# Kernel tuning notes

Measured on AMD Instinct MI355X. Metric: run time of the kernel, lower is better.

## Reference

```python
import jax, jax.numpy as jnp
import numpy as np

KW = 3          # kernel_width
PAD = (KW - 1) // 2


def setup_inputs() -> dict:
    key = jax.random.key(0)
    ks = jax.random.split(key, 7)
    B, Lq, Lk, D, C = 8, 1024, 1024, 512, 512  # D=q_size, C=k_size
    return {
        "q": jax.random.normal(ks[0], (B, Lq, D), jnp.float32),
        "k": jax.random.normal(ks[1], (B, Lk, C), jnp.float32),
        "W_kernel": jax.random.normal(ks[2], (D, C * KW), jnp.float32) * (1.0 / np.sqrt(D)),
        "b_kernel": jax.random.normal(ks[3], (C * KW,), jnp.float32) * 0.02,
        "W_bias": jax.random.normal(ks[4], (D, 1), jnp.float32) * (1.0 / np.sqrt(D)),
        "b_bias": jax.random.normal(ks[5], (1,), jnp.float32) * 0.02,
        "bias_b": jax.random.normal(ks[6], (1,), jnp.float32),
    }


def reference(q, k, W_kernel, b_kernel, W_bias, b_bias, bias_b):
    B, Lq, D = q.shape
    _, Lk, C = k.shape
    # per-(batch, query) dynamic conv kernels: [B, Lq, C, KW]
    kernel = (q @ W_kernel + b_kernel).reshape(B, Lq, C, KW)
    # per-(batch, query) scalar bias: [B, Lq]
    bias = (q @ W_bias + b_bias)[..., 0]
    # windowed view of k (cross-correlation with 'same' padding)
    kpad = jnp.pad(k, ((0, 0), (PAD, PAD), (0, 0)))  # [B, Lk+2*PAD, C]
    win_idx = jnp.arange(Lk)[:, None] + jnp.arange(KW)[None, :]  # [Lk, KW]
    kwin = kpad[:, win_idx, :]  # [B, Lk, KW, C]
    # a[b,i,j] = sum_{c,w} kernel[b,i,c,w] * kpad[b, j+w, c] + bias[b,i] + bias_b
    a_ij = jnp.einsum('bicw,bjwc->bij', kernel, kwin)
    return a_ij + bias[:, :, None] + bias_b
```

## Files before the change

kernel.cpp:

```cpp
#include <hip/hip_runtime.h>


typedef __attribute__((ext_vector_type(8))) short s8vec;
typedef __attribute__((ext_vector_type(4))) float floatx4;

__device__ __forceinline__ unsigned short f2bf(float f) {
    union { float f; unsigned u; } v; v.f = f;
    unsigned r = (v.u + 0x7FFFu + ((v.u >> 16) & 1u)) >> 16;
    return (unsigned short)r;
}

__device__ __forceinline__ void gl2lds16(const void* g, void* l) {
    __builtin_amdgcn_global_load_lds(
        (__attribute__((address_space(1))) void*)(g),
        (__attribute__((address_space(3))) void*)(l), 16, 0, 0);
}

__global__ void cvt_all(const float* __restrict__ q, const float* __restrict__ k,
                        unsigned short* __restrict__ qbf, unsigned short* __restrict__ kp,
                        const float* __restrict__ Wb, const float* __restrict__ b_bias,
                        float* __restrict__ biasb,
                        const float* __restrict__ W, unsigned short* __restrict__ Wt) {
    int blk = blockIdx.x;
    if (blk < 4104) {
        int t = blk * 256 + threadIdx.x;
        if (t < 524288) {
            const float4* p = (const float4*)q + 2 * (size_t)t;
            float4 a = p[0], b = p[1];
            union { unsigned short s[8]; uint4 v; } o;
            o.s[0]=f2bf(a.x); o.s[1]=f2bf(a.y); o.s[2]=f2bf(a.z); o.s[3]=f2bf(a.w);
            o.s[4]=f2bf(b.x); o.s[5]=f2bf(b.y); o.s[6]=f2bf(b.z); o.s[7]=f2bf(b.w);
            ((uint4*)qbf)[t] = o.v;
        } else if (t < 1048576) {
            int e8 = t - 524288;
            size_t e = (size_t)e8 * 8;
            int b = e8 >> 16;
            int j = (e8 >> 6) & 1023;
            int c = (e8 & 63) * 8;
            const float4* p = (const float4*)(k + e);
            float4 a = p[0], bb = p[1];
            union { unsigned short s[8]; uint4 v; } o;
            o.s[0]=f2bf(a.x); o.s[1]=f2bf(a.y); o.s[2]=f2bf(a.z); o.s[3]=f2bf(a.w);
            o.s[4]=f2bf(bb.x); o.s[5]=f2bf(bb.y); o.s[6]=f2bf(bb.z); o.s[7]=f2bf(bb.w);
            *(uint4*)(kp + ((size_t)(b * 1028 + j + 1) * 512 + c)) = o.v;
        } else if (t < 1050624) {
            int z = t - 1048576;
            int b = z >> 8, r = (z >> 6) & 3, ch = z & 63;
            int row = r ? (1024 + r) : 0;
            *(uint4*)(kp + ((size_t)(b * 1028 + row) * 512 + ch * 8)) = make_uint4(0u,0u,0u,0u);
        }
    } else if (blk < 6152) {
        int row  = (blk - 4104) * 4 + (threadIdx.x >> 6);
        int lane = threadIdx.x & 63;
        const float4* qr = (const float4*)(q + (size_t)row * 512) + lane * 2;
        const float4* wb = (const float4*)Wb + lane * 2;
        float4 a0 = qr[0], a1 = qr[1], b0 = wb[0], b1 = wb[1];
        float s = a0.x*b0.x + a0.y*b0.y + a0.z*b0.z + a0.w*b0.w
                + a1.x*b1.x + a1.y*b1.y + a1.z*b1.z + a1.w*b1.w;
        #pragma unroll
        for (int off = 32; off > 0; off >>= 1) s += __shfl_down(s, off);
        if (lane == 0) biasb[row] = s + b_bias[0];
    } else {
        __shared__ float lds[32][33];
        int p = blk - 6152;
        int cw0 = (p % 48) * 32, d0 = (p / 48) * 32;
        int tid = threadIdx.x;
        #pragma unroll
        for (int rep = 0; rep < 4; rep++) {
            int e = rep * 256 + tid, dy = e >> 5, dx = e & 31;
            lds[dy][dx] = W[(size_t)(d0 + dy) * 1536 + cw0 + dx];
        }
        __syncthreads();
        #pragma unroll
        for (int rep = 0; rep < 4; rep++) {
            int e = rep * 256 + tid, cy = e >> 5, cx = e & 31;
            int cw = cw0 + cy, c = cw / 3, w = cw % 3;
            Wt[((size_t)(w * 512 + c)) * 512 + d0 + cx] = f2bf(lds[cx][cy]);
        }
    }
}

__global__ __launch_bounds__(256) void gemm_A(const unsigned short* __restrict__ Abf,
                                              const unsigned short* __restrict__ Bbf,
                                              const float* __restrict__ b_kernel,
                                              unsigned short* __restrict__ G) {
    __shared__ unsigned short lds_a[128 * 32];
    __shared__ unsigned short lds_b[128 * 32];
    int g = blockIdx.x;
    int xcd = g & 7, slot = g >> 3;
    int n_blk = slot / 8;
    int i_blk = xcd * 8 + (slot & 7);
    int i0 = i_blk * 128;
    int n0 = n_blk * 128;
    int tid = threadIdx.x, wid = tid >> 6, lane = tid & 63;
    int wm = wid >> 1, wn = wid & 1;
    floatx4 acc[4][4] = {};

    for (int kk = 0; kk < 512; kk += 32) {
        #pragma unroll
        for (int s = 0; s < 2; ++s) {
            int t = wid * 2 + s;
            const unsigned short* ga = Abf + (size_t)(i0 + t * 16 + (lane >> 2)) * 512 + kk + (lane & 3) * 8;
            gl2lds16(ga, (char*)lds_a + t * 1024);
            const unsigned short* gb = Bbf + (size_t)(n0 + t * 16 + (lane >> 2)) * 512 + kk + (lane & 3) * 8;
            gl2lds16(gb, (char*)lds_b + t * 1024);
        }
        __syncthreads();
        int ra = lane & 15, q8 = (lane >> 4) * 8;
        s8vec af[4], bf_[4];
        #pragma unroll
        for (int mi = 0; mi < 4; mi++)
            af[mi] = *(const s8vec*)(lds_a + (wm * 64 + mi * 16 + ra) * 32 + q8);
        #pragma unroll
        for (int ni = 0; ni < 4; ni++)
            bf_[ni] = *(const s8vec*)(lds_b + (wn * 64 + ni * 16 + ra) * 32 + q8);
        #pragma unroll
        for (int mi = 0; mi < 4; mi++)
            #pragma unroll
            for (int ni = 0; ni < 4; ni++)
                acc[mi][ni] = __builtin_amdgcn_mfma_f32_16x16x32_bf16(af[mi], bf_[ni], acc[mi][ni], 0, 0, 0);
        __syncthreads();
    }

    int cl = lane & 15, qd = lane >> 4;
    #pragma unroll
    for (int mi = 0; mi < 4; mi++) {
        #pragma unroll
        for (int ni = 0; ni < 4; ni++) {
            int n_all = n0 + wn * 64 + ni * 16 + cl;
            int c = n_all & 511, w = n_all >> 9;
            float bk = b_kernel[c * 3 + w];
            #pragma unroll
            for (int r = 0; r < 4; r++) {
                int i_g = i0 + wm * 64 + mi * 16 + qd * 4 + r;
                int b = i_g >> 10, ii = i_g & 1023;
                G[((size_t)((b * 3 + w) * 1024 + ii)) * 512 + c] = f2bf(acc[mi][ni][r] + bk);
            }
        }
    }
}

__global__ __launch_bounds__(256) void gemm_B(const unsigned short* __restrict__ G,
                                              const unsigned short* __restrict__ kp,
                                              const float* __restrict__ biasb,
                                              const float* __restrict__ bias_b,
                                              float* __restrict__ out) {
    __shared__ unsigned short lds_a[3 * 64 * 32];
    __shared__ unsigned short lds_k[272 * 32];
    int g = blockIdx.x;
    int b = g & 7, slot = g >> 3;
    int j0 = (slot & 3) * 256;
    int i0 = (slot >> 2) * 64;
    int tid = threadIdx.x, wid = tid >> 6, lane = tid & 63;
    floatx4 acc[4][4] = {};
    const unsigned short* Gb  = G  + (size_t)b * 3 * 1024 * 512;
    const unsigned short* kpb = kp + (size_t)b * 1028 * 512;
    float bb = bias_b[0];

    for (int kk = 0; kk < 512; kk += 32) {
        #pragma unroll
        for (int s2 = 0; s2 < 8; ++s2) {
            int t = s2 * 4 + wid;
            if (t < 29) {
                if (t < 12) {
                    int w = t >> 2, chunk = t & 3;
                    const unsigned short* ga = Gb + (size_t)(w * 1024 + i0 + chunk * 16 + (lane >> 2)) * 512
                                                  + kk + (lane & 3) * 8;
                    gl2lds16(ga, (char*)lds_a + t * 1024);
                } else {
                    int u = t - 12;
                    const unsigned short* gk = kpb + (size_t)(j0 + u * 16 + (lane >> 2)) * 512
                                                   + kk + (lane & 3) * 8;
                    gl2lds16(gk, (char*)lds_k + u * 1024);
                }
            }
        }
        __syncthreads();
        int ra = lane & 15, q8 = (lane >> 4) * 8;
        #pragma unroll
        for (int w = 0; w < 3; ++w) {
            s8vec af[4], bfr[4];
            #pragma unroll
            for (int mi = 0; mi < 4; mi++)
                af[mi] = *(const s8vec*)(lds_a + (w * 64 + mi * 16 + ra) * 32 + q8);
            #pragma unroll
            for (int ni = 0; ni < 4; ni++) {
                int rr = wid * 64 + ni * 16 + ra + w;
                bfr[ni] = *(const s8vec*)(lds_k + rr * 32 + q8);
            }
            #pragma unroll
            for (int mi = 0; mi < 4; mi++)
                #pragma unroll
                for (int ni = 0; ni < 4; ni++)
                    acc[mi][ni] = __builtin_amdgcn_mfma_f32_16x16x32_bf16(af[mi], bfr[ni], acc[mi][ni], 0, 0, 0);
        }
        __syncthreads();
    }

    int cl = lane & 15, qd = lane >> 4;
    #pragma unroll
    for (int mi = 0; mi < 4; mi++) {
        #pragma unroll
        for (int r = 0; r < 4; r++) {
            int i_loc = mi * 16 + qd * 4 + r;
            float bv = biasb[b * 1024 + i0 + i_loc] + bb;
            float* orow = out + ((size_t)(b * 1024 + i0 + i_loc)) * 1024 + j0;
            #pragma unroll
            for (int ni = 0; ni < 4; ni++) {
                int j_loc = wid * 64 + ni * 16 + cl;
                orow[j_loc] = acc[mi][ni][r] + bv;
            }
        }
    }
}

extern "C" void kernel_launch(void* const* d_in, const int* in_sizes, int n_in,
                              void* d_out, int out_size, void* d_ws, size_t ws_size,
                              hipStream_t stream) {
    const float* q        = (const float*)d_in[0];
    const float* k        = (const float*)d_in[1];
    const float* W_kernel = (const float*)d_in[2];
    const float* b_kernel = (const float*)d_in[3];
    const float* W_bias   = (const float*)d_in[4];
    const float* b_bias   = (const float*)d_in[5];
    const float* bias_b   = (const float*)d_in[6];
    float* out = (float*)d_out;

    char* ws = (char*)d_ws;
    unsigned short* q_bf = (unsigned short*)(ws);
    unsigned short* kp   = (unsigned short*)(ws + 8388608);
    unsigned short* Wt   = (unsigned short*)(ws + 8388608 + 8421376 + 16384);
    unsigned short* G    = (unsigned short*)(ws + 8388608 + 8421376 + 16384 + 1572864);
    float*          bsb  = (float*)(ws + 8388608 + 8421376 + 16384 + 1572864 + 25165824);

    cvt_all<<<6920, 256, 0, stream>>>(q, k, q_bf, kp, W_bias, b_bias, bsb, W_kernel, Wt);
    gemm_A<<<768, 256, 0, stream>>>(q_bf, Wt, b_kernel, G);
    gemm_B<<<512, 256, 0, stream>>>(G, kp, bsb, bias_b, out);
}
```

Baseline: 142.4 us.

## Reassociate dynamic conv attention: precompute K·W^T then single Q·V GEMM

Reorders the contraction so the per-key projection V[b,j,d] = sum_{c,w} kpad[b,j+w,c]*W[d,c,w] is computed first. The output then becomes a plain batched q·V^T GEMM plus per-row and per-column bias terms, where the b_kernel contribution is a separate per-key vector tj. This removes the large 3x-wide intermediate G and the three-tap inner GEMM. The cost is an extra GEMM over K=1536 on the keys and a new bias-reduction pass, and V is rounded to bf16, which may change numerical error.

Measured after the change: 170.5 us. 19.7% more time.

```diff
diff --git a/kernel.cpp b/kernel.cpp
--- a/kernel.cpp
+++ b/kernel.cpp
@@ -19,8 +19,9 @@
 __global__ void cvt_all(const float* __restrict__ q, const float* __restrict__ k,
                         unsigned short* __restrict__ qbf, unsigned short* __restrict__ kp,
                         const float* __restrict__ Wb, const float* __restrict__ b_bias,
-                        float* __restrict__ biasb,
-                        const float* __restrict__ W, unsigned short* __restrict__ Wt) {
+                        float* __restrict__ biasq,
+                        const float* __restrict__ W, unsigned short* __restrict__ Wt2,
+                        const float* __restrict__ b_kernel, float* __restrict__ tj) {
     int blk = blockIdx.x;
     if (blk < 4104) {
         int t = blk * 256 + threadIdx.x;
@@ -59,156 +60,163 @@
                 + a1.x*b1.x + a1.y*b1.y + a1.z*b1.z + a1.w*b1.w;
         #pragma unroll
         for (int off = 32; off > 0; off >>= 1) s += __shfl_down(s, off);
-        if (lane == 0) biasb[row] = s + b_bias[0];
+        if (lane == 0) biasq[row] = s + b_bias[0];
+    } else if (blk < 6536) {
+        int e = (blk - 6152) * 256 + threadIdx.x;
+        int d = e / 192;
+        int rem = e - d * 192;
+        int w = rem >> 6, c0 = (rem & 63) * 8;
+        const float* wrow = W + (size_t)d * 1536;
+        union { unsigned short s[8]; uint4 v; } o;
+        #pragma unroll
+        for (int i = 0; i < 8; i++) o.s[i] = f2bf(wrow[(c0 + i) * 3 + w]);
+        *(uint4*)(Wt2 + (size_t)d * 1536 + w * 512 + c0) = o.v;
     } else {
-        __shared__ float lds[32][33];
-        int p = blk - 6152;
-        int cw0 = (p % 48) * 32, d0 = (p / 48) * 32;
-        int tid = threadIdx.x;
-        #pragma unroll
-        for (int rep = 0; rep < 4; rep++) {
-            int e = rep * 256 + tid, dy = e >> 5, dx = e & 31;
-            lds[dy][dx] = W[(size_t)(d0 + dy) * 1536 + cw0 + dx];
-        }
-        __syncthreads();
-        #pragma unroll
-        for (int rep = 0; rep < 4; rep++) {
-            int e = rep * 256 + tid, cy = e >> 5, cx = e & 31;
-            int cw = cw0 + cy, c = cw / 3, w = cw % 3;
-            Wt[((size_t)(w * 512 + c)) * 512 + d0 + cx] = f2bf(lds[cx][cy]);
-        }
-    }
-}
-
-__global__ __launch_bounds__(256) void gemm_A(const unsigned short* __restrict__ Abf,
-                                              const unsigned short* __restrict__ Bbf,
-                                              const float* __restrict__ b_kernel,
-                                              unsigned short* __restrict__ G) {
+        int row  = (blk - 6536) * 4 + (threadIdx.x >> 6);
+        int lane = threadIdx.x & 63;
+        int b = row >> 10, j = row & 1023;
+        int c0 = lane * 8;
+        const float* kb = k + (size_t)b * 1024 * 512;
+        float s = 0.0f;
+        #pragma unroll
+        for (int w = 0; w < 3; w++) {
+            int r = j + w - 1;
+            if (r >= 0 && r < 1024) {
+                const float4* kr = (const float4*)(kb + (size_t)r * 512) + lane * 2;
+                float4 a0 = kr[0], a1 = kr[1];
+                const float* bk = b_kernel + w;
+                s += a0.x * bk[(c0+0)*3] + a0.y * bk[(c0+1)*3]
+                   + a0.z * bk[(c0+2)*3] + a0.w * bk[(c0+3)*3]
+                   + a1.x * bk[(c0+4)*3] + a1.y * bk[(c0+5)*3]
+                   + a1.z * bk[(c0+6)*3] + a1.w * bk[(c0+7)*3];
+            }
+        }
+        #pragma unroll
+        for (int off = 32; off > 0; off >>= 1) s += __shfl_down(s, off);
+        if (lane == 0) tj[row] = s;
+    }
+}
+
+__global__ __launch_bounds__(256) void gemm_V(const unsigned short* __restrict__ kp,
+                                              const unsigned short* __restrict__ Wt2,
+                                              unsigned short* __restrict__ V) {
+    __shared__ unsigned short lds_a[128 * 32];
+    __shared__ unsigned short lds_b[64 * 32];
+    int g = blockIdx.x;
+    int b = g & 7, slot = g >> 3;
+    int j0 = (slot >> 3) * 128;
+    int n0 = (slot & 7) * 64;
+    int tid = threadIdx.x, wid = tid >> 6, lane = tid & 63;
+    int wm = wid >> 1, wn = wid & 1;
+    const unsigned short* kpb = kp + (size_t)(b * 1028 + j0) * 512;
+    floatx4 acc[4][2] = {};
+
+    for (int kk = 0; kk < 1536; kk += 32) {
+        #pragma unroll
+        for (int s = 0; s < 3; ++s) {
+            int t = wid * 3 + s;
+            if (t < 8) {
+                const unsigned short* ga = kpb + (size_t)(t * 16 + (lane >> 2)) * 512 + kk + (lane & 3) * 8;
+                gl2lds16(ga, (char*)lds_a + t * 1024);
+            } else {
+                int u = t - 8;
+                const unsigned short* gb = Wt2 + (size_t)(n0 + u * 16 + (lane >> 2)) * 1536 + kk + (lane & 3) * 8;
+                gl2lds16(gb, (char*)lds_b + u * 1024);
+            }
+        }
+        __syncthreads();
+        int ra = lane & 15, q8 = (lane >> 4) * 8;
+        s8vec af[4], bfr[2];
+        #pragma unroll
+        for (int mi = 0; mi < 4; mi++)
+            af[mi] = *(const s8vec*)(lds_a + (wm * 64 + mi * 16 + ra) * 32 + q8);
+        #pragma unroll
+        for (int ni = 0; ni < 2; ni++)
+            bfr[ni] = *(const s8vec*)(lds_b + (wn * 32 + ni * 16 + ra) * 32 + q8);
+        #pragma unroll
+        for (int mi = 0; mi < 4; mi++)
+            #pragma unroll
+            for (int ni = 0; ni < 2; ni++)
+                acc[mi][ni] = __builtin_amdgcn_mfma_f32_16x16x32_bf16(af[mi], bfr[ni], acc[mi][ni], 0, 0, 0);
+        __syncthreads();
+    }
+
+    int cl = lane & 15, qd = lane >> 4;
+    #pragma unroll
+    for (int mi = 0; mi < 4; mi++) {
+        #pragma unroll
+        for (int ni = 0; ni < 2; ni++) {
+            int col = n0 + wn * 32 + ni * 16 + cl;
+            #pragma unroll
+            for (int r = 0; r < 4; r++) {
+                int m_g = b * 1024 + j0 + wm * 64 + mi * 16 + qd * 4 + r;
+                V[(size_t)m_g * 512 + col] = f2bf(acc[mi][ni][r]);
+            }
+        }
+    }
+}
+
+__global__ __launch_bounds__(256) void gemm_QV(const unsigned short* __restrict__ qbf,
+                                               const unsigned short* __restrict__ V,
+                                               const float* __restrict__ biasq,
+                                               const float* __restrict__ tj,
+                                               const float* __restrict__ bias_b,
+                                               float* __restrict__ out) {
     __shared__ unsigned short lds_a[128 * 32];
     __shared__ unsigned short lds_b[128 * 32];
     int g = blockIdx.x;
-    int xcd = g & 7, slot = g >> 3;
-    int n_blk = slot / 8;
-    int i_blk = xcd * 8 + (slot & 7);
-    int i0 = i_blk * 128;
-    int n0 = n_blk * 128;
+    int b = g & 7, slot = g >> 3;
+    int i0 = (slot >> 3) * 128;
+    int j0 = (slot & 7) * 128;
     int tid = threadIdx.x, wid = tid >> 6, lane = tid & 63;
     int wm = wid >> 1, wn = wid & 1;
+    const unsigned short* Ab = qbf + (size_t)b * 1024 * 512;
+    const unsigned short* Bb = V   + (size_t)b * 1024 * 512;
     floatx4 acc[4][4] = {};
 
     for (int kk = 0; kk < 512; kk += 32) {
         #pragma unroll
         for (int s = 0; s < 2; ++s) {
             int t = wid * 2 + s;
-            const unsigned short* ga = Abf + (size_t)(i0 + t * 16 + (lane >> 2)) * 512 + kk + (lane & 3) * 8;
+            const unsigned short* ga = Ab + (size_t)(i0 + t * 16 + (lane >> 2)) * 512 + kk + (lane & 3) * 8;
             gl2lds16(ga, (char*)lds_a + t * 1024);
-            const unsigned short* gb = Bbf + (size_t)(n0 + t * 16 + (lane >> 2)) * 512 + kk + (lane & 3) * 8;
+            const unsigned short* gb = Bb + (size_t)(j0 + t * 16 + (lane >> 2)) * 512 + kk + (lane & 3) * 8;
             gl2lds16(gb, (char*)lds_b + t * 1024);
         }
         __syncthreads();
         int ra = lane & 15, q8 = (lane >> 4) * 8;
-        s8vec af[4], bf_[4];
+        s8vec af[4], bfr[4];
         #pragma unroll
         for (int mi = 0; mi < 4; mi++)
             af[mi] = *(const s8vec*)(lds_a + (wm * 64 + mi * 16 + ra) * 32 + q8);
         #pragma unroll
         for (int ni = 0; ni < 4; ni++)
-            bf_[ni] = *(const s8vec*)(lds_b + (wn * 64 + ni * 16 + ra) * 32 + q8);
+            bfr[ni] = *(const s8vec*)(lds_b + (wn * 64 + ni * 16 + ra) * 32 + q8);
         #pragma unroll
         for (int mi = 0; mi < 4; mi++)
             #pragma unroll
             for (int ni = 0; ni < 4; ni++)
-                acc[mi][ni] = __builtin_amdgcn_mfma_f32_16x16x32_bf16(af[mi], bf_[ni], acc[mi][ni], 0, 0, 0);
+                acc[mi][ni] = __builtin_amdgcn_mfma_f32_16x16x32_bf16(af[mi], bfr[ni], acc[mi][ni], 0, 0, 0);
         __syncthreads();
     }
 
     int cl = lane & 15, qd = lane >> 4;
+    float bb = bias_b[0];
+    float tv[4];
+    #pragma unroll
+    for (int ni = 0; ni < 4; ni++)
+        tv[ni] = tj[b * 1024 + j0 + wn * 64 + ni * 16 + cl];
     #pragma unroll
     for (int mi = 0; mi < 4; mi++) {
         #pragma unroll
-        for (int ni = 0; ni < 4; ni++) {
-            int n_all = n0 + wn * 64 + ni * 16 + cl;
-            int c = n_all & 511, w = n_all >> 9;
-            float bk = b_kernel[c * 3 + w];
-            #pragma unroll
-            for (int r = 0; r < 4; r++) {
-                int i_g = i0 + wm * 64 + mi * 16 + qd * 4 + r;
-                int b = i_g >> 10, ii = i_g & 1023;
-                G[((size_t)((b * 3 + w) * 1024 + ii)) * 512 + c] = f2bf(acc[mi][ni][r] + bk);
-            }
-        }
-    }
-}
-
-__global__ __launch_bounds__(256) void gemm_B(const unsigned short* __restrict__ G,
-                                              const unsigned short* __restrict__ kp,
-                                              const float* __restrict__ biasb,
-                                              const float* __restrict__ bias_b,
-                                              float* __restrict__ out) {
-    __shared__ unsigned short lds_a[3 * 64 * 32];
-    __shared__ unsigned short lds_k[272 * 32];
-    int g = blockIdx.x;
-    int b = g & 7, slot = g >> 3;
-    int j0 = (slot & 3) * 256;
-    int i0 = (slot >> 2) * 64;
-    int tid = threadIdx.x, wid = tid >> 6, lane = tid & 63;
-    floatx4 acc[4][4] = {};
-    const unsigned short* Gb  = G  + (size_t)b * 3 * 1024 * 512;
-    const unsigned short* kpb = kp + (size_t)b * 1028 * 512;
-    float bb = bias_b[0];
-
-    for (int kk = 0; kk < 512; kk += 32) {
-        #pragma unroll
-        for (int s2 = 0; s2 < 8; ++s2) {
-            int t = s2 * 4 + wid;
-            if (t < 29) {
-                if (t < 12) {
-                    int w = t >> 2, chunk = t & 3;
-                    const unsigned short* ga = Gb + (size_t)(w * 1024 + i0 + chunk * 16 + (lane >> 2)) * 512
-                                                  + kk + (lane & 3) * 8;
-                    gl2lds16(ga, (char*)lds_a + t * 1024);
-                } else {
-                    int u = t - 12;
-                    const unsigned short* gk = kpb + (size_t)(j0 + u * 16 + (lane >> 2)) * 512
-                                                   + kk + (lane & 3) * 8;
-                    gl2lds16(gk, (char*)lds_k + u * 1024);
-                }
-            }
-        }
-        __syncthreads();
-        int ra = lane & 15, q8 = (lane >> 4) * 8;
-        #pragma unroll
-        for (int w = 0; w < 3; ++w) {
-            s8vec af[4], bfr[4];
-            #pragma unroll
-            for (int mi = 0; mi < 4; mi++)
-                af[mi] = *(const s8vec*)(lds_a + (w * 64 + mi * 16 + ra) * 32 + q8);
+        for (int r = 0; r < 4; r++) {
+            int i_g = i0 + wm * 64 + mi * 16 + qd * 4 + r;
+            float bv = biasq[b * 1024 + i_g] + bb;
+            float* orow = out + ((size_t)(b * 1024 + i_g)) * 1024 + j0;
             #pragma unroll
             for (int ni = 0; ni < 4; ni++) {
-                int rr = wid * 64 + ni * 16 + ra + w;
-                bfr[ni] = *(const s8vec*)(lds_k + rr * 32 + q8);
-            }
-            #pragma unroll
-            for (int mi = 0; mi < 4; mi++)
-                #pragma unroll
-                for (int ni = 0; ni < 4; ni++)
-                    acc[mi][ni] = __builtin_amdgcn_mfma_f32_16x16x32_bf16(af[mi], bfr[ni], acc[mi][ni], 0, 0, 0);
-        }
-        __syncthreads();
-    }
-
-    int cl = lane & 15, qd = lane >> 4;
-    #pragma unroll
-    for (int mi = 0; mi < 4; mi++) {
-        #pragma unroll
-        for (int r = 0; r < 4; r++) {
-            int i_loc = mi * 16 + qd * 4 + r;
-            float bv = biasb[b * 1024 + i0 + i_loc] + bb;
-            float* orow = out + ((size_t)(b * 1024 + i0 + i_loc)) * 1024 + j0;
-            #pragma unroll
-            for (int ni = 0; ni < 4; ni++) {
-                int j_loc = wid * 64 + ni * 16 + cl;
-                orow[j_loc] = acc[mi][ni][r] + bv;
+                int j_loc = wn * 64 + ni * 16 + cl;
+                orow[j_loc] = acc[mi][ni][r] + bv + tv[ni];
             }
         }
     }
@@ -229,11 +237,12 @@
     char* ws = (char*)d_ws;
     unsigned short* q_bf = (unsigned short*)(ws);
     unsigned short* kp   = (unsigned short*)(ws + 8388608);
-    unsigned short* Wt   = (unsigned short*)(ws + 8388608 + 8421376 + 16384);
-    unsigned short* G    = (unsigned short*)(ws + 8388608 + 8421376 + 16384 + 1572864);
-    float*          bsb  = (float*)(ws + 8388608 + 8421376 + 16384 + 1572864 + 25165824);
-
-    cvt_all<<<6920, 256, 0, stream>>>(q, k, q_bf, kp, W_bias, b_bias, bsb, W_kernel, Wt);
-    gemm_A<<<768, 256, 0, stream>>>(q_bf, Wt, b_kernel, G);
-    gemm_B<<<512, 256, 0, stream>>>(G, kp, bsb, bias_b, out);
-}
+    unsigned short* Wt2  = (unsigned short*)(ws + 8388608 + 8421376 + 16384);
+    unsigned short* V    = (unsigned short*)(ws + 8388608 + 8421376 + 16384 + 1572864);
+    float*          bsq  = (float*)(ws + 8388608 + 8421376 + 16384 + 1572864 + 8388608);
+    float*          tj   = (float*)(ws + 8388608 + 8421376 + 16384 + 1572864 + 8388608 + 32768);
+
+    cvt_all<<<8584, 256, 0, stream>>>(q, k, q_bf, kp, W_bias, b_bias, bsq, W_kernel, Wt2, b_kernel, tj);
+    gemm_V<<<512, 256, 0, stream>>>(kp, Wt2, V);
+    gemm_QV<<<512, 256, 0, stream>>>(q_bf, V, bsq, tj, bias_b, out);
+}
```
